# Kernel tuning notes

Measured on AMD Instinct MI355X. Metric: run time of the kernel, lower is better.

The kernel has to match this reference:

```python
import jax, jax.numpy as jnp
import numpy as np

C1, C2, C3 = 64, 256, 256
HEADS, WS = 8, 7
HD = C3 // HEADS
PAD = WS // 2
SCALE = HD ** -0.5
EPS = 1e-5


def _layernorm(x, gamma, beta):
    mu = jnp.mean(x, axis=-1, keepdims=True)
    var = jnp.var(x, axis=-1, keepdims=True)
    return (x - mu) * jax.lax.rsqrt(var + EPS) * gamma + beta


def setup_inputs() -> dict:
    key = jax.random.key(0)
    ks = jax.random.split(key, 12)
    B, H, W = 2, 200, 200
    s = 0.02
    return {
        "F_lidar": jax.random.normal(ks[0], (B, C1, H, W), jnp.float32),
        "F_cam": jax.random.normal(ks[1], (B, C2, H, W), jnp.float32),
        "Wq": jax.random.normal(ks[2], (C3, C1), jnp.float32) * s,
        "Wk": jax.random.normal(ks[3], (C3, C2), jnp.float32) * s,
        "Wv": jax.random.normal(ks[4], (C3, C2), jnp.float32) * s,
        "Wo": jax.random.normal(ks[5], (C3, C3), jnp.float32) * s,
        "Wr": jax.random.normal(ks[6], (C3, C1), jnp.float32) * s,
        "g1": jnp.ones((C3,), jnp.float32),
        "b1": jnp.zeros((C3,), jnp.float32),
        "g2": jnp.ones((C3,), jnp.float32),
        "b2": jnp.zeros((C3,), jnp.float32),
        "W1": jax.random.normal(ks[7], (C3, 4 * C3), jnp.float32) * s,
        "bf1": jnp.zeros((4 * C3,), jnp.float32),
        "W2": jax.random.normal(ks[8], (4 * C3, C3), jnp.float32) * s,
        "bf2": jnp.zeros((C3,), jnp.float32),
    }


def reference(F_lidar, F_cam, Wq, Wk, Wv, Wo, Wr, g1, b1, g2, b2, W1, bf1, W2, bf2):
    B, _, H, W = F_lidar.shape
    # 1x1 conv projections (no bias)
    Q = jnp.einsum('oc,bchw->bohw', Wq, F_lidar)
    K = jnp.einsum('oc,bchw->bohw', Wk, F_cam)
    V = jnp.einsum('oc,bchw->bohw', Wv, F_cam)
    # replicate padding (torch 'replicate' == jnp 'edge')
    Kp = jnp.pad(K, ((0, 0), (0, 0), (PAD, PAD), (PAD, PAD)), mode='edge')
    Vp = jnp.pad(V, ((0, 0), (0, 0), (PAD, PAD), (PAD, PAD)), mode='edge')
    Qm = Q.reshape(B, HEADS, HD, H, W)
    # local-window attention logits without materializing the unfolded (C*49) tensor:
    # loop over the 49 fixed window offsets, accumulating per-offset dot products.
    logits = []
    for i in range(WS):
        for j in range(WS):
            Km = Kp[:, :, i:i + H, j:j + W].reshape(B, HEADS, HD, H, W)
            logits.append(jnp.einsum('bndhw,bndhw->bnhw', Qm, Km))
    logits = jnp.stack(logits, axis=-1) * SCALE          # (B, heads, H, W, 49)
    attn = jax.nn.softmax(logits, axis=-1)
    out = jnp.zeros_like(Qm)
    k = 0
    for i in range(WS):
        for j in range(WS):
            Vm = Vp[:, :, i:i + H, j:j + W].reshape(B, HEADS, HD, H, W)
            out = out + attn[..., k][:, :, None] * Vm
            k += 1
    out = out.reshape(B, C3, H, W)
    out = jnp.einsum('oc,bchw->bohw', Wo, out)
    residual = jnp.einsum('oc,bchw->bohw', Wr, F_lidar)
    x = (residual + out).transpose(0, 2, 3, 1)           # (B, H, W, C3)
    x = _layernorm(x, g1, b1)
    # FFN (dropout is identity in eval)
    y = jax.nn.relu(jnp.dot(x, W1) + bf1)
    y = jnp.dot(y, W2) + bf2
    x = _layernorm(x + y, g2, b2)
    return x.transpose(0, 3, 1, 2)
```

## Files before the change

kernel.cpp:

```cpp
#include <hip/hip_runtime.h>
#include <stdint.h>

#define HH 200
#define WW 200
#define HWSZ 40000
#define NPX 80000

typedef __attribute__((ext_vector_type(8))) short bf16x8;
typedef __attribute__((ext_vector_type(4))) float f32x4;

#define VM_WAIT(N) asm volatile("s_waitcnt vmcnt(" #N ")" ::: "memory")
#define LGKM_WAIT0 asm volatile("s_waitcnt lgkmcnt(0)" ::: "memory")
#define BARRIER()  __builtin_amdgcn_s_barrier()
#define SCHED_FENCE() __builtin_amdgcn_sched_barrier(0)

__device__ __forceinline__ float bf2f(unsigned short u) {
    union { uint32_t i; float f; } c; c.i = ((uint32_t)u) << 16; return c.f;
}
__device__ __forceinline__ unsigned short f2bf(float f) {
    union { float f; uint32_t i; } c; c.f = f;
    uint32_t r = c.i + 0x7FFF + ((c.i >> 16) & 1);
    return (unsigned short)(r >> 16);
}
__device__ __forceinline__ unsigned int cvtpk_bf16(float lo, float hi) {
    unsigned int r;
    asm("v_cvt_pk_bf16_f32 %0, %1, %2" : "=v"(r) : "v"(lo), "v"(hi));
    return r;
}
__device__ __forceinline__ void gload16(const void* g, void* l) {
    __builtin_amdgcn_global_load_lds(
        (const __attribute__((address_space(1))) unsigned int*)g,
        (__attribute__((address_space(3))) unsigned int*)l, 16, 0, 0);
}

__global__ __launch_bounds__(256) void cvt_weights(
    const float* __restrict__ Wq, const float* __restrict__ Wk,
    const float* __restrict__ Wv, const float* __restrict__ Wo,
    const float* __restrict__ Wr, const float* __restrict__ W1,
    const float* __restrict__ W2,
    unsigned short* Wq_b, unsigned short* Wk_b, unsigned short* Wv_b,
    unsigned short* Wcat, unsigned short* W1t, unsigned short* W2t)
{
    const int seg = blockIdx.y;
    const int idx = blockIdx.x * 256 + threadIdx.x;
    if (seg == 0)      { if (idx < 16384) Wq_b[idx] = f2bf(Wq[idx]); }
    else if (seg == 1) { if (idx < 65536) Wk_b[idx] = f2bf(Wk[idx]); }
    else if (seg == 2) { if (idx < 65536) Wv_b[idx] = f2bf(Wv[idx]); }
    else if (seg == 3) {
        if (idx < 81920) {
            int r = idx / 320, k = idx - r * 320;
            Wcat[idx] = f2bf(k < 256 ? Wo[r * 256 + k] : Wr[r * 64 + (k - 256)]);
        }
    } else if (seg == 4) {
        if (idx < 262144) { int o = idx >> 8, i = idx & 255; W1t[idx] = f2bf(W1[i * 1024 + o]); }
    } else {
        if (idx < 262144) { int o = idx >> 10, i = idx & 1023; W2t[idx] = f2bf(W2[i * 256 + o]); }
    }
}

__global__ __launch_bounds__(256) void to_nhwc(
    const float* __restrict__ src, unsigned short* __restrict__ dst, int C)
{
    __shared__ unsigned short T[64][72];
    const int b = blockIdx.z, c0 = blockIdx.y * 64, px0 = blockIdx.x * 64;
    const int t = threadIdx.x;
    const int pxl = t & 63, cl0 = t >> 6;
    const float* sp = src + ((size_t)(b * C + c0 + cl0)) * HWSZ + px0 + pxl;
    #pragma unroll
    for (int i = 0; i < 16; ++i)
        T[pxl][cl0 + i * 4] = f2bf(sp[(size_t)i * 4 * HWSZ]);
    __syncthreads();
    #pragma unroll
    for (int r = 0; r < 2; ++r) {
        int idx = t + r * 256;
        int p = idx >> 3, cof = (idx & 7) * 8;
        uint4 v = *(const uint4*)&T[p][cof];
        *(uint4*)(dst + ((size_t)(b * HWSZ + px0 + p)) * C + c0 + cof) = v;
    }
}

__global__ __launch_bounds__(256) void gemm_bf16(
    const unsigned short* __restrict__ In, int inStride,
    const unsigned short* __restrict__ In2, int in2Stride, int K1,
    const unsigned short* __restrict__ Wb, int wStride, int Ktot,
    unsigned short* __restrict__ OutB, float* __restrict__ OutF,
    const float* __restrict__ bias, int flags, int outStride)
{
    __shared__ bf16x8 AB[2][1024];
    const int t = threadIdx.x;
    int bx = blockIdx.x, by = blockIdx.y;
    if (flags & 4) {
        const int nxy = gridDim.x * gridDim.y;
        const int flat = blockIdx.x + gridDim.x * blockIdx.y;
        const int qq = nxy >> 3, rr = nxy & 7;
        const int xcd = flat & 7, idx = flat >> 3;
        const int w2 = (xcd < rr ? xcd * (qq + 1)
                                 : rr * (qq + 1) + (xcd - rr) * qq) + idx;
        by = w2 % gridDim.y;
        bx = w2 / gridDim.y;
    }
    const int px0 = bx * 128;
    const int n0 = by * 128;
    const int lane = t & 63, w = t >> 6;
    const int mh = w & 1, nh = w >> 1;

    f32x4 acc[4][4] = {};

    auto STAGE = [&](int buf, int k0s) {
        #pragma unroll
        for (int r = 0; r < 2; ++r) {
            const int c = t + r * 256;
            const int l = c & 63;
            const int ko = k0s + ((l >> 4) << 3);
            const int mt = c >> 6;
            {
                const int px = px0 + mt * 16 + (l & 15);
                const unsigned short* sp = (ko < K1)
                    ? (In  + (size_t)px * inStride  + ko)
                    : (In2 + (size_t)px * in2Stride + (ko - K1));
                gload16(sp, &AB[buf][c]);
            }
            {
                const int cc = n0 + mt * 16 + (l & 15);
                gload16(Wb + (size_t)cc * wStride + ko, &AB[buf][512 + c]);
            }
        }
    };

    const int nsteps = Ktot >> 5;
    STAGE(0, 0);
    if (nsteps > 1) STAGE(1, 32);
    int cur = 0;

    for (int s = 0; s < nsteps - 1; ++s) {
        VM_WAIT(4);
        BARRIER();
        bf16x8 av[4], bv[4];
        #pragma unroll
        for (int i = 0; i < 4; ++i) av[i] = AB[cur][(mh * 4 + i) * 64 + lane];
        #pragma unroll
        for (int j = 0; j < 4; ++j) bv[j] = AB[cur][512 + (nh * 4 + j) * 64 + lane];
        LGKM_WAIT0;
        BARRIER();
        SCHED_FENCE();
        if (s + 2 < nsteps) STAGE(cur, (s + 2) * 32);
        #pragma unroll
        for (int i = 0; i < 4; ++i)
            #pragma unroll
            for (int j = 0; j < 4; ++j)
                acc[i][j] = __builtin_amdgcn_mfma_f32_16x16x32_bf16(
                    av[i], bv[j], acc[i][j], 0, 0, 0);
        cur ^= 1;
    }
    VM_WAIT(0);
    BARRIER();
    {
        bf16x8 av[4], bv[4];
        #pragma unroll
        for (int i = 0; i < 4; ++i) av[i] = AB[cur][(mh * 4 + i) * 64 + lane];
        #pragma unroll
        for (int j = 0; j < 4; ++j) bv[j] = AB[cur][512 + (nh * 4 + j) * 64 + lane];
        #pragma unroll
        for (int i = 0; i < 4; ++i)
            #pragma unroll
            for (int j = 0; j < 4; ++j)
                acc[i][j] = __builtin_amdgcn_mfma_f32_16x16x32_bf16(
                    av[i], bv[j], acc[i][j], 0, 0, 0);
    }

    const int q = lane >> 4, ln = lane & 15;
    const bool relu = (flags & 1) != 0, accum = (flags & 2) != 0;
    #pragma unroll
    for (int i = 0; i < 4; ++i) {
        #pragma unroll
        for (int j = 0; j < 4; ++j) {
            const int coutv = n0 + nh * 64 + j * 16 + ln;
            const float bval = bias ? bias[coutv] : 0.0f;
            #pragma unroll
            for (int r = 0; r < 4; ++r) {
                const int px = px0 + mh * 64 + i * 16 + q * 4 + r;
                float v = acc[i][j][r] + bval;
                if (relu) v = fmaxf(v, 0.0f);
                if (OutB) {
                    OutB[(size_t)px * outStride + coutv] = f2bf(v);
                } else {
                    float* op = OutF + (size_t)px * 256 + coutv;
                    if (accum) v += *op;
                    *op = v;
                }
            }
        }
    }
}

__global__ __launch_bounds__(512) void ffn2_ln2(
    const unsigned short* __restrict__ Y1,
    const unsigned short* __restrict__ XLb,
    const unsigned short* __restrict__ W2t,
    const float* __restrict__ bf2v,
    const float* __restrict__ g2, const float* __restrict__ b2,
    float* __restrict__ Out)
{
    __shared__ union {
        bf16x8 AB[2][1536];
        float  T[256 * 33];
    } sm;
    __shared__ float part_s[4][128], part_q[4][128];

    const int t = threadIdx.x;
    const int px0 = blockIdx.x * 128;
    const int lane = t & 63, w = t >> 6;
    const int mh = w & 1, nh = w >> 1;
    const int q = lane >> 4, ln = lane & 15;

    float biasv[4], gv[4], bvv[4];
    #pragma unroll
    for (int j = 0; j < 4; ++j) {
        const int col = nh * 64 + j * 16 + ln;
        biasv[j] = bf2v[col];
        gv[j] = g2[col];
        bvv[j] = b2[col];
    }

    f32x4 acc[4][4] = {};

    auto STAGE = [&](int buf, int k0s) {
        #pragma unroll
        for (int r = 0; r < 3; ++r) {
            const int c = t + r * 512;
            const int l = c & 63;
            const int ko = k0s + ((l >> 4) << 3);
            if (c < 512) {
                const int mt = c >> 6;
                const int px = px0 + mt * 16 + (l & 15);
                gload16(Y1 + (size_t)px * 1024 + ko, &sm.AB[buf][c]);
            } else {
                const int c2 = c - 512;
                const int nt = c2 >> 6;
                const int cc = nt * 16 + (l & 15);
                gload16(W2t + (size_t)cc * 1024 + ko, &sm.AB[buf][c]);
            }
        }
    };

    STAGE(0, 0);
    STAGE(1, 32);
    int cur = 0;

    for (int s = 0; s < 31; ++s) {
        VM_WAIT(3);
        BARRIER();
        bf16x8 av[4], bv[4];
        #pragma unroll
        for (int i = 0; i < 4; ++i) av[i] = sm.AB[cur][(mh * 4 + i) * 64 + lane];
        #pragma unroll
        for (int j = 0; j < 4; ++j) bv[j] = sm.AB[cur][512 + (nh * 4 + j) * 64 + lane];
        LGKM_WAIT0;
        BARRIER();
        SCHED_FENCE();
        if (s + 2 < 32) STAGE(cur, (s + 2) * 32);
        #pragma unroll
        for (int i = 0; i < 4; ++i)
            #pragma unroll
            for (int j = 0; j < 4; ++j)
                acc[i][j] = __builtin_amdgcn_mfma_f32_16x16x32_bf16(
                    av[i], bv[j], acc[i][j], 0, 0, 0);
        cur ^= 1;
    }
    VM_WAIT(0);
    BARRIER();
    {
        bf16x8 av[4], bv[4];
        #pragma unroll
        for (int i = 0; i < 4; ++i) av[i] = sm.AB[cur][(mh * 4 + i) * 64 + lane];
        #pragma unroll
        for (int j = 0; j < 4; ++j) bv[j] = sm.AB[cur][512 + (nh * 4 + j) * 64 + lane];
        #pragma unroll
        for (int i = 0; i < 4; ++i)
            #pragma unroll
            for (int j = 0; j < 4; ++j)
                acc[i][j] = __builtin_amdgcn_mfma_f32_16x16x32_bf16(
                    av[i], bv[j], acc[i][j], 0, 0, 0);
    }

    #pragma unroll
    for (int i = 0; i < 4; ++i) {
        #pragma unroll
        for (int r = 0; r < 4; ++r) {
            const int pl = mh * 64 + i * 16 + q * 4 + r;
            const size_t px = (size_t)px0 + pl;
            float s = 0.0f, ssq = 0.0f;
            #pragma unroll
            for (int j = 0; j < 4; ++j) {
                const int col = nh * 64 + j * 16 + ln;
                float v = acc[i][j][r] + biasv[j] + bf2f(XLb[px * 256 + col]);
                acc[i][j][r] = v;
                s += v; ssq += v * v;
            }
            #pragma unroll
            for (int o = 1; o <= 8; o <<= 1) {
                s += __shfl_xor(s, o); ssq += __shfl_xor(ssq, o);
            }
            if (ln == 0) { part_s[nh][pl] = s; part_q[nh][pl] = ssq; }
        }
    }
    __syncthreads();

    float muv[4][4], rsv[4][4];
    #pragma unroll
    for (int i = 0; i < 4; ++i) {
        #pragma unroll
        for (int r = 0; r < 4; ++r) {
            const int pl = mh * 64 + i * 16 + q * 4 + r;
            const float s  = part_s[0][pl] + part_s[1][pl] + part_s[2][pl] + part_s[3][pl];
            const float sq = part_q[0][pl] + part_q[1][pl] + part_q[2][pl] + part_q[3][pl];
            const float mu = s * (1.0f / 256.0f);
            muv[i][r] = mu;
            rsv[i][r] = rsqrtf(sq * (1.0f / 256.0f) - mu * mu + 1e-5f);
        }
    }
    __syncthreads();

    #pragma unroll
    for (int ck = 0; ck < 4; ++ck) {
        if (mh == (ck >> 1)) {
            const int ib = (ck & 1) * 2;
            #pragma unroll
            for (int ii = 0; ii < 2; ++ii) {
                const int i = ib + ii;
                #pragma unroll
                for (int j = 0; j < 4; ++j) {
                    const int col = nh * 64 + j * 16 + ln;
                    #pragma unroll
                    for (int r = 0; r < 4; ++r) {
                        sm.T[col * 33 + ii * 16 + q * 4 + r] =
                            (acc[i][j][r] - muv[i][r]) * rsv[i][r] * gv[j] + bvv[j];
                    }
                }
            }
        }
        __syncthreads();
        const int pxc = px0 + ck * 32;
        const int bb = pxc / HWSZ;
        const int hw0 = pxc - bb * HWSZ;
        #pragma unroll
        for (int p = 0; p < 16; ++p) {
            const int idx = t + p * 512;
            const int c = idx >> 5, pxl = idx & 31;
            Out[((size_t)(bb * 256 + c)) * HWSZ + hw0 + pxl] = sm.T[c * 33 + pxl];
        }
        __syncthreads();
    }
}

__global__ __launch_bounds__(256) void attn_bf16(
    const unsigned short* Q, const unsigned short* __restrict__ K,
    const unsigned short* __restrict__ V, unsigned short* A)
{
    __shared__ __align__(16) unsigned short vt[32 * 536];
    const int flat = blockIdx.x + 169 * (blockIdx.y + 8 * blockIdx.z);
    const int wsz = (flat & 7) * 338 + (flat >> 3);
    const int tile = wsz >> 4, rem = wsz & 15;
    const int head = rem >> 1, b = rem & 1;
    const int tiy = tile / 13, tix = tile - tiy * 13;
    const int h0 = tiy * 16, w0 = tix * 16;
    const int t = threadIdx.x;
    const int lane = t & 63, wv = t >> 6;
    const int g = lane >> 4, n = lane & 15;
    const int co = head * 32;
    const size_t pxb = (size_t)b * HWSZ;

    for (int idx = t; idx < 832; idx += 256) {
        if (idx < 704) {
            int ch = idx / 22, r = idx - ch * 22;
            *(unsigned int*)&vt[ch * 536 + r * 24 + 22] = 0u;
        } else {
            int k2 = idx - 704;
            int ch = k2 >> 2, e = k2 & 3;
            *(unsigned int*)&vt[ch * 536 + 528 + e * 2] = 0u;
        }
    }
    for (int idx = t; idx < 484 * 4; idx += 256) {
        int pos = idx >> 2, chunk = idx & 3;
        int r = pos / 22, c = pos - r * 22;
        int gh = min(max(h0 + r - 3, 0), HH - 1);
        int gw = min(max(w0 + c - 3, 0), WW - 1);
        bf16x8 v8 = *(const bf16x8*)(V + (pxb + gh * WW + gw) * 256 + co + chunk * 8);
        unsigned short* dp = &vt[(chunk * 8) * 536 + r * 24 + c];
        #pragma unroll
        for (int e = 0; e < 8; ++e) dp[e * 536] = (unsigned short)v8[e];
    }
    __syncthreads();

    const f32x4 z4 = {0.f, 0.f, 0.f, 0.f};
    const int qw  = min(w0 + n, WW - 1);
    const int kc0 = min(max(w0 - 3 + n, 0), WW - 1);
    const int kc1 = min(w0 + 13 + n, WW - 1);
    const bool hi2 = (g >> 1) != 0;
    const int src0 = ((g & 1) * 2) * 16 + n;
    const int src1 = src0 + 16;

    for (int hh = 0; hh < 4; ++hh) {
        const int hl = wv * 4 + hh;
        const int h = h0 + hl;
        const int hc = min(h, HH - 1);

        const bf16x8 qf = *(const bf16x8*)(Q + (pxb + hc * WW + qw) * 256 + co + g * 8);

        f32x4 s0[7], s1[7];
        #pragma unroll
        for (int i = 0; i < 7; ++i) {
            const int gh = min(max(h - 3 + i, 0), HH - 1);
            const unsigned short* kr = K + (pxb + gh * WW) * 256 + co + g * 8;
            bf16x8 a0 = *(const bf16x8*)(kr + (size_t)kc0 * 256);
            bf16x8 a1 = *(const bf16x8*)(kr + (size_t)kc1 * 256);
            s0[i] = __builtin_amdgcn_mfma_f32_16x16x32_bf16(a0, qf, z4, 0, 0, 0);
            s1[i] = __builtin_amdgcn_mfma_f32_16x16x32_bf16(a1, qf, z4, 0, 0, 0);
        }

        float mx = -3.0e38f;
        #pragma unroll
        for (int r = 0; r < 4; ++r) {
            float m0 = s0[0][r], m1 = s1[0][r];
            #pragma unroll
            for (int i = 1; i < 7; ++i) {
                m0 = fmaxf(m0, s0[i][r]);
                m1 = fmaxf(m1, s1[i][r]);
            }
            const int k0 = 4 * g + r, k1 = k0 + 16;
            mx = fmaxf(mx, ((unsigned)(k0 - n) <= 6u) ? m0 : -3.0e38f);
            mx = fmaxf(mx, ((unsigned)(k1 - n) <= 6u) ? m1 : -3.0e38f);
        }
        mx = fmaxf(mx, __shfl_xor(mx, 16));
        mx = fmaxf(mx, __shfl_xor(mx, 32));

        float sum = 0.0f;
        #pragma unroll
        for (int r = 0; r < 4; ++r) {
            const int k0 = 4 * g + r, k1 = k0 + 16;
            const bool in0 = (unsigned)(k0 - n) <= 6u;
            const bool in1 = (unsigned)(k1 - n) <= 6u;
            #pragma unroll
            for (int i = 0; i < 7; ++i) {
                float e0 = in0 ? __expf((s0[i][r] - mx) * 0.17677669529663687f) : 0.0f;
                float e1 = in1 ? __expf((s1[i][r] - mx) * 0.17677669529663687f) : 0.0f;
                s0[i][r] = e0; s1[i][r] = e1;
                sum += e0 + e1;
            }
        }
        sum += __shfl_xor(sum, 16);
        sum += __shfl_xor(sum, 32);
        const float inv = __builtin_amdgcn_rcpf(sum);

        unsigned int pa[7], pb[7], pc[7], pd[7];
        #pragma unroll
        for (int i = 0; i < 7; ++i) {
            pa[i] = cvtpk_bf16(s0[i][0] * inv, s0[i][1] * inv);
            pb[i] = cvtpk_bf16(s0[i][2] * inv, s0[i][3] * inv);
            pc[i] = cvtpk_bf16(s1[i][0] * inv, s1[i][1] * inv);
            pd[i] = cvtpk_bf16(s1[i][2] * inv, s1[i][3] * inv);
        }

        f32x4 acc0 = z4, acc1 = z4;
        #pragma unroll
        for (int i = 0; i < 7; ++i) {
            const int a0s = __shfl((int)pa[i], src0);
            const int c0s = __shfl((int)pc[i], src0);
            const int b0s = __shfl((int)pb[i], src0);
            const int d0s = __shfl((int)pd[i], src0);
            const int a1s = __shfl((int)pa[i], src1);
            const int c1s = __shfl((int)pc[i], src1);
            const int b1s = __shfl((int)pb[i], src1);
            const int d1s = __shfl((int)pd[i], src1);
            union { unsigned int u[4]; bf16x8 v; } pu;
            pu.u[0] = (unsigned int)(hi2 ? c0s : a0s);
            pu.u[1] = (unsigned int)(hi2 ? d0s : b0s);
            pu.u[2] = (unsigned int)(hi2 ? c1s : a1s);
            pu.u[3] = (unsigned int)(hi2 ? d1s : b1s);
            const unsigned short* vr = &vt[(hl + i) * 24 + g * 8];
            bf16x8 vf0 = *(const bf16x8*)(vr + n * 536);
            bf16x8 vf1 = *(const bf16x8*)(vr + (n + 16) * 536);
            acc0 = __builtin_amdgcn_mfma_f32_16x16x32_bf16(pu.v, vf0, acc0, 0, 0, 0);
            acc1 = __builtin_amdgcn_mfma_f32_16x16x32_bf16(pu.v, vf1, acc1, 0, 0, 0);
        }

        if (h < HH) {
            unsigned short* ap = A + (pxb + h * WW) * 256 + co + n;
            const int wp = w0 + g * 4;
            #pragma unroll
            for (int r = 0; r < 4; ++r) {
                if (wp + r < WW) {
                    ap[(size_t)(wp + r) * 256]      = f2bf(acc0[r]);
                    ap[(size_t)(wp + r) * 256 + 16] = f2bf(acc1[r]);
                }
            }
        }
    }
}

__global__ __launch_bounds__(256) void ln1_k(
    const float* __restrict__ X, const float* __restrict__ g,
    const float* __restrict__ bt, unsigned short* __restrict__ XLb)
{
    const int wv = threadIdx.x >> 6, lane = threadIdx.x & 63;
    const size_t px = (size_t)blockIdx.x * 4 + wv;
    const float4 v = *(const float4*)(X + px * 256 + lane * 4);
    float s = v.x + v.y + v.z + v.w;
    float ss = v.x * v.x + v.y * v.y + v.z * v.z + v.w * v.w;
    #pragma unroll
    for (int o = 32; o; o >>= 1) { s += __shfl_xor(s, o); ss += __shfl_xor(ss, o); }
    const float mu = s * (1.0f / 256.0f);
    const float var = ss * (1.0f / 256.0f) - mu * mu;
    const float rs = rsqrtf(var + 1e-5f);
    const float4 gv = *(const float4*)(g + lane * 4);
    const float4 bv = *(const float4*)(bt + lane * 4);
    ushort4 o4;
    o4.x = f2bf((v.x - mu) * rs * gv.x + bv.x);
    o4.y = f2bf((v.y - mu) * rs * gv.y + bv.y);
    o4.z = f2bf((v.z - mu) * rs * gv.z + bv.z);
    o4.w = f2bf((v.w - mu) * rs * gv.w + bv.w);
    *(ushort4*)(XLb + px * 256 + lane * 4) = o4;
}

extern "C" void kernel_launch(void* const* d_in, const int* in_sizes, int n_in,
                              void* d_out, int out_size, void* d_ws, size_t ws_size,
                              hipStream_t stream)
{
    const float* F_lidar = (const float*)d_in[0];
    const float* F_cam   = (const float*)d_in[1];
    const float* Wq  = (const float*)d_in[2];
    const float* Wk  = (const float*)d_in[3];
    const float* Wv  = (const float*)d_in[4];
    const float* Wo  = (const float*)d_in[5];
    const float* Wr  = (const float*)d_in[6];
    const float* g1  = (const float*)d_in[7];
    const float* b1  = (const float*)d_in[8];
    const float* g2  = (const float*)d_in[9];
    const float* b2  = (const float*)d_in[10];
    const float* W1  = (const float*)d_in[11];
    const float* bf1 = (const float*)d_in[12];
    const float* W2  = (const float*)d_in[13];
    const float* bf2 = (const float*)d_in[14];

    char* wsb = (char*)d_ws;
    unsigned short* Fl  = (unsigned short*)(wsb);
    unsigned short* Fc  = (unsigned short*)(wsb + 10240000);
    unsigned short* Qb  = (unsigned short*)(wsb + 51200000);
    unsigned short* Kb  = (unsigned short*)(wsb + 92160000);
    unsigned short* Vb  = (unsigned short*)(wsb + 133120000);
    unsigned short* Y1b = Fc;
    unsigned short* XLb = (unsigned short*)(wsb + 174080000);
    unsigned short* Wq_b = (unsigned short*)(wsb + 215040000);
    unsigned short* Wk_b = Wq_b + 16384;
    unsigned short* Wv_b = Wk_b + 65536;
    unsigned short* Wcat = Wv_b + 65536;
    unsigned short* W1t  = Wcat + 81920;
    unsigned short* W2t  = W1t + 262144;
    float* XW  = (float*)d_out;
    float* out = (float*)d_out;

    const dim3 blk(256);

    cvt_weights<<<dim3(1024, 6), blk, 0, stream>>>(Wq, Wk, Wv, Wo, Wr, W1, W2,
        Wq_b, Wk_b, Wv_b, Wcat, W1t, W2t);
    to_nhwc<<<dim3(625, 1, 2), blk, 0, stream>>>(F_lidar, Fl, 64);
    to_nhwc<<<dim3(625, 4, 2), blk, 0, stream>>>(F_cam, Fc, 256);

    gemm_bf16<<<dim3(625, 2), blk, 0, stream>>>(Fl, 64, Fl, 64, 64,
        Wq_b, 64, 64, Qb, nullptr, nullptr, 4, 256);
    gemm_bf16<<<dim3(625, 2), blk, 0, stream>>>(Fc, 256, Fc, 256, 256,
        Wk_b, 256, 256, Kb, nullptr, nullptr, 4, 256);
    gemm_bf16<<<dim3(625, 2), blk, 0, stream>>>(Fc, 256, Fc, 256, 256,
        Wv_b, 256, 256, Vb, nullptr, nullptr, 4, 256);

    attn_bf16<<<dim3(169, 8, 2), blk, 0, stream>>>(Qb, Kb, Vb, Qb);

    gemm_bf16<<<dim3(625, 2), blk, 0, stream>>>(Qb, 256, Fl, 64, 256,
        Wcat, 320, 320, nullptr, XW, nullptr, 4, 256);

    ln1_k<<<dim3(20000), blk, 0, stream>>>(XW, g1, b1, XLb);

    gemm_bf16<<<dim3(625, 8), blk, 0, stream>>>(XLb, 256, XLb, 256, 256,
        W1t, 256, 256, Y1b, nullptr, bf1, 5, 1024);

    ffn2_ln2<<<dim3(625), dim3(512), 0, stream>>>(Y1b, XLb, W2t, bf2, g2, b2, out);
}
```

Baseline: 682.5 us.

## Fuse K/V projections into one GEMM and fuse output projection with LayerNorm1

Concatenates Wk and Wv into one weight matrix so a single GEMM launch computes both K and V, splitting output columns into separate buffers. Replaces the output-projection GEMM plus standalone ln1 kernel with a proj_ln1 kernel that computes the full 256-column row per block and applies LayerNorm in registers via cross-wave partial sums. This removes the fp32 intermediate write and read of the projection result and two launches. In exchange, the fused kernel uses 512 threads with a larger LDS footprint, which may lower occupancy.

```diff
diff --git a/kernel.cpp b/kernel.cpp
--- a/kernel.cpp
+++ b/kernel.cpp
@@ -38,20 +38,23 @@
     const float* __restrict__ Wv, const float* __restrict__ Wo,
     const float* __restrict__ Wr, const float* __restrict__ W1,
     const float* __restrict__ W2,
-    unsigned short* Wq_b, unsigned short* Wk_b, unsigned short* Wv_b,
+    unsigned short* Wq_b, unsigned short* Wkv_b,
     unsigned short* Wcat, unsigned short* W1t, unsigned short* W2t)
 {
     const int seg = blockIdx.y;
     const int idx = blockIdx.x * 256 + threadIdx.x;
     if (seg == 0)      { if (idx < 16384) Wq_b[idx] = f2bf(Wq[idx]); }
-    else if (seg == 1) { if (idx < 65536) Wk_b[idx] = f2bf(Wk[idx]); }
-    else if (seg == 2) { if (idx < 65536) Wv_b[idx] = f2bf(Wv[idx]); }
-    else if (seg == 3) {
+    else if (seg == 1) {
+        if (idx < 131072) {
+            int r = idx >> 8, k = idx & 255;
+            Wkv_b[idx] = f2bf(r < 256 ? Wk[r * 256 + k] : Wv[(r - 256) * 256 + k]);
+        }
+    } else if (seg == 2) {
         if (idx < 81920) {
             int r = idx / 320, k = idx - r * 320;
             Wcat[idx] = f2bf(k < 256 ? Wo[r * 256 + k] : Wr[r * 64 + (k - 256)]);
         }
-    } else if (seg == 4) {
+    } else if (seg == 3) {
         if (idx < 262144) { int o = idx >> 8, i = idx & 255; W1t[idx] = f2bf(W1[i * 1024 + o]); }
     } else {
         if (idx < 262144) { int o = idx >> 10, i = idx & 1023; W2t[idx] = f2bf(W2[i * 256 + o]); }
@@ -83,7 +86,8 @@
     const unsigned short* __restrict__ In, int inStride,
     const unsigned short* __restrict__ In2, int in2Stride, int K1,
     const unsigned short* __restrict__ Wb, int wStride, int Ktot,
-    unsigned short* __restrict__ OutB, float* __restrict__ OutF,
+    unsigned short* __restrict__ OutB, unsigned short* __restrict__ OutB2,
+    float* __restrict__ OutF,
     const float* __restrict__ bias, int flags, int outStride)
 {
     __shared__ bf16x8 AB[2][1024];
@@ -170,6 +174,7 @@
 
     const int q = lane >> 4, ln = lane & 15;
     const bool relu = (flags & 1) != 0, accum = (flags & 2) != 0;
+    const bool split = (flags & 8) != 0;
     #pragma unroll
     for (int i = 0; i < 4; ++i) {
         #pragma unroll
@@ -182,12 +187,142 @@
                 float v = acc[i][j][r] + bval;
                 if (relu) v = fmaxf(v, 0.0f);
                 if (OutB) {
-                    OutB[(size_t)px * outStride + coutv] = f2bf(v);
+                    if (split && coutv >= 256)
+                        OutB2[(size_t)px * outStride + coutv - 256] = f2bf(v);
+                    else
+                        OutB[(size_t)px * outStride + coutv] = f2bf(v);
                 } else {
                     float* op = OutF + (size_t)px * 256 + coutv;
                     if (accum) v += *op;
                     *op = v;
                 }
+            }
+        }
+    }
+}
+
+__global__ __launch_bounds__(512) void proj_ln1(
+    const unsigned short* __restrict__ Aq,
+    const unsigned short* __restrict__ Fl,
+    const unsigned short* __restrict__ Wcat,
+    const float* __restrict__ g1, const float* __restrict__ b1,
+    unsigned short* __restrict__ XLb)
+{
+    __shared__ bf16x8 AB[2][1536];
+    __shared__ float part_s[4][128], part_q[4][128];
+
+    const int t = threadIdx.x;
+    const int px0 = blockIdx.x * 128;
+    const int lane = t & 63, w = t >> 6;
+    const int mh = w & 1, nh = w >> 1;
+    const int q = lane >> 4, ln = lane & 15;
+
+    float gv[4], bvv[4];
+    #pragma unroll
+    for (int j = 0; j < 4; ++j) {
+        const int col = nh * 64 + j * 16 + ln;
+        gv[j] = g1[col];
+        bvv[j] = b1[col];
+    }
+
+    f32x4 acc[4][4] = {};
+
+    auto STAGE = [&](int buf, int k0s) {
+        #pragma unroll
+        for (int r = 0; r < 3; ++r) {
+            const int c = t + r * 512;
+            const int l = c & 63;
+            const int ko = k0s + ((l >> 4) << 3);
+            if (c < 512) {
+                const int mt = c >> 6;
+                const int px = px0 + mt * 16 + (l & 15);
+                const unsigned short* sp = (ko < 256)
+                    ? (Aq + (size_t)px * 256 + ko)
+                    : (Fl + (size_t)px * 64 + (ko - 256));
+                gload16(sp, &AB[buf][c]);
+            } else {
+                const int c2 = c - 512;
+                const int nt = c2 >> 6;
+                const int cc = nt * 16 + (l & 15);
+                gload16(Wcat + (size_t)cc * 320 + ko, &AB[buf][c]);
+            }
+        }
+    };
+
+    STAGE(0, 0);
+    STAGE(1, 32);
+    int cur = 0;
+
+    for (int s = 0; s < 9; ++s) {
+        VM_WAIT(3);
+        BARRIER();
+        bf16x8 av[4], bv[4];
+        #pragma unroll
+        for (int i = 0; i < 4; ++i) av[i] = AB[cur][(mh * 4 + i) * 64 + lane];
+        #pragma unroll
+        for (int j = 0; j < 4; ++j) bv[j] = AB[cur][512 + (nh * 4 + j) * 64 + lane];
+        LGKM_WAIT0;
+        BARRIER();
+        SCHED_FENCE();
+        if (s + 2 < 10) STAGE(cur, (s + 2) * 32);
+        #pragma unroll
+        for (int i = 0; i < 4; ++i)
+            #pragma unroll
+            for (int j = 0; j < 4; ++j)
+                acc[i][j] = __builtin_amdgcn_mfma_f32_16x16x32_bf16(
+                    av[i], bv[j], acc[i][j], 0, 0, 0);
+        cur ^= 1;
+    }
+    VM_WAIT(0);
+    BARRIER();
+    {
+        bf16x8 av[4], bv[4];
+        #pragma unroll
+        for (int i = 0; i < 4; ++i) av[i] = AB[cur][(mh * 4 + i) * 64 + lane];
+        #pragma unroll
+        for (int j = 0; j < 4; ++j) bv[j] = AB[cur][512 + (nh * 4 + j) * 64 + lane];
+        #pragma unroll
+        for (int i = 0; i < 4; ++i)
+            #pragma unroll
+            for (int j = 0; j < 4; ++j)
+                acc[i][j] = __builtin_amdgcn_mfma_f32_16x16x32_bf16(
+                    av[i], bv[j], acc[i][j], 0, 0, 0);
+    }
+
+    #pragma unroll
+    for (int i = 0; i < 4; ++i) {
+        #pragma unroll
+        for (int r = 0; r < 4; ++r) {
+            const int pl = mh * 64 + i * 16 + q * 4 + r;
+            float s = 0.0f, ssq = 0.0f;
+            #pragma unroll
+            for (int j = 0; j < 4; ++j) {
+                const float v = acc[i][j][r];
+                s += v; ssq += v * v;
+            }
+            #pragma unroll
+            for (int o = 1; o <= 8; o <<= 1) {
+                s += __shfl_xor(s, o); ssq += __shfl_xor(ssq, o);
+            }
+            if (ln == 0) { part_s[nh][pl] = s; part_q[nh][pl] = ssq; }
+        }
+    }
+    __syncthreads();
+
+    #pragma unroll
+    for (int i = 0; i < 4; ++i) {
+        #pragma unroll
+        for (int r = 0; r < 4; ++r) {
+            const int pl = mh * 64 + i * 16 + q * 4 + r;
+            const size_t px = (size_t)px0 + pl;
+            const float s  = part_s[0][pl] + part_s[1][pl] + part_s[2][pl] + part_s[3][pl];
+            const float sq = part_q[0][pl] + part_q[1][pl] + part_q[2][pl] + part_q[3][pl];
+            const float mu = s * (1.0f / 256.0f);
+            const float rs = rsqrtf(sq * (1.0f / 256.0f) - mu * mu + 1e-5f);
+            #pragma unroll
+            for (int j = 0; j < 4; ++j) {
+                const int col = nh * 64 + j * 16 + ln;
+                XLb[px * 256 + col] = f2bf((acc[i][j][r] - mu) * rs * gv[j] + bvv[j]);
             }
         }
     }
@@ -498,30 +633,6 @@
     }
 }
 
-__global__ __launch_bounds__(256) void ln1_k(
-    const float* __restrict__ X, const float* __restrict__ g,
-    const float* __restrict__ bt, unsigned short* __restrict__ XLb)
-{
-    const int wv = threadIdx.x >> 6, lane = threadIdx.x & 63;
-    const size_t px = (size_t)blockIdx.x * 4 + wv;
-    const float4 v = *(const float4*)(X + px * 256 + lane * 4);
-    float s = v.x + v.y + v.z + v.w;
-    float ss = v.x * v.x + v.y * v.y + v.z * v.z + v.w * v.w;
-    #pragma unroll
-    for (int o = 32; o; o >>= 1) { s += __shfl_xor(s, o); ss += __shfl_xor(ss, o); }
-    const float mu = s * (1.0f / 256.0f);
-    const float var = ss * (1.0f / 256.0f) - mu * mu;
-    const float rs = rsqrtf(var + 1e-5f);
-    const float4 gv = *(const float4*)(g + lane * 4);
-    const float4 bv = *(const float4*)(bt + lane * 4);
-    ushort4 o4;
-    o4.x = f2bf((v.x - mu) * rs * gv.x + bv.x);
-    o4.y = f2bf((v.y - mu) * rs * gv.y + bv.y);
-    o4.z = f2bf((v.z - mu) * rs * gv.z + bv.z);
-    o4.w = f2bf((v.w - mu) * rs * gv.w + bv.w);
-    *(ushort4*)(XLb + px * 256 + lane * 4) = o4;
-}
-
 extern "C" void kernel_launch(void* const* d_in, const int* in_sizes, int n_in,
                               void* d_out, int out_size, void* d_ws, size_t ws_size,
                               hipStream_t stream)
@@ -550,38 +661,31 @@
     unsigned short* Vb  = (unsigned short*)(wsb + 133120000);
     unsigned short* Y1b = Fc;
     unsigned short* XLb = (unsigned short*)(wsb + 174080000);
-    unsigned short* Wq_b = (unsigned short*)(wsb + 215040000);
-    unsigned short* Wk_b = Wq_b + 16384;
-    unsigned short* Wv_b = Wk_b + 65536;
-    unsigned short* Wcat = Wv_b + 65536;
-    unsigned short* W1t  = Wcat + 81920;
-    unsigned short* W2t  = W1t + 262144;
-    float* XW  = (float*)d_out;
+    unsigned short* Wq_b  = (unsigned short*)(wsb + 215040000);
+    unsigned short* Wkv_b = Wq_b + 16384;
+    unsigned short* Wcat  = Wkv_b + 131072;
+    unsigned short* W1t   = Wcat + 81920;
+    unsigned short* W2t   = W1t + 262144;
     float* out = (float*)d_out;
 
     const dim3 blk(256);
 
-    cvt_weights<<<dim3(1024, 6), blk, 0, stream>>>(Wq, Wk, Wv, Wo, Wr, W1, W2,
-        Wq_b, Wk_b, Wv_b, Wcat, W1t, W2t);
+    cvt_weights<<<dim3(1024, 5), blk, 0, stream>>>(Wq, Wk, Wv, Wo, Wr, W1, W2,
+        Wq_b, Wkv_b, Wcat, W1t, W2t);
     to_nhwc<<<dim3(625, 1, 2), blk, 0, stream>>>(F_lidar, Fl, 64);
     to_nhwc<<<dim3(625, 4, 2), blk, 0, stream>>>(F_cam, Fc, 256);
 
     gemm_bf16<<<dim3(625, 2), blk, 0, stream>>>(Fl, 64, Fl, 64, 64,
-        Wq_b, 64, 64, Qb, nullptr, nullptr, 4, 256);
-    gemm_bf16<<<dim3(625, 2), blk, 0, stream>>>(Fc, 256, Fc, 256, 256,
-        Wk_b, 256, 256, Kb, nullptr, nullptr, 4, 256);
-    gemm_bf16<<<dim3(625, 2), blk, 0, stream>>>(Fc, 256, Fc, 256, 256,
-        Wv_b, 256, 256, Vb, nullptr, nullptr, 4, 256);
+        Wq_b, 64, 64, Qb, nullptr, nullptr, nullptr, 4, 256);
+    gemm_bf16<<<dim3(625, 4), blk, 0, stream>>>(Fc, 256, Fc, 256, 256,
+        Wkv_b, 256, 256, Kb, Vb, nullptr, nullptr, 4 | 8, 256);
 
     attn_bf16<<<dim3(169, 8, 2), blk, 0, stream>>>(Qb, Kb, Vb, Qb);
 
-    gemm_bf16<<<dim3(625, 2), blk, 0, stream>>>(Qb, 256, Fl, 64, 256,
-        Wcat, 320, 320, nullptr, XW, nullptr, 4, 256);
-
-    ln1_k<<<dim3(20000), blk, 0, stream>>>(XW, g1, b1, XLb);
+    proj_ln1<<<dim3(625), dim3(512), 0, stream>>>(Qb, Fl, Wcat, g1, b1, XLb);
 
     gemm_bf16<<<dim3(625, 8), blk, 0, stream>>>(XLb, 256, XLb, 256, 256,
-        W1t, 256, 256, Y1b, nullptr, bf1, 5, 1024);
+        W1t, 256, 256, Y1b, nullptr, nullptr, bf1, 5, 1024);
 
     ffn2_ln2<<<dim3(625), dim3(512), 0, stream>>>(Y1b, XLb, W2t, bf2, g2, b2, out);
 }
```

New measurement: 650.6 us. -4.7%, faster.
